# Kernel tuning notes

Measured on AMD Instinct MI355X. Metric: run time of the kernel, lower is better.

## Reference

```python
import jax, jax.numpy as jnp
import numpy as np


def setup_inputs() -> dict:
    key = jax.random.key(0)
    k1, k2, k3 = jax.random.split(key, 3)
    B, S, D, L = 8, 512, 512, 32
    head = jax.random.normal(k1, (B, S, D), dtype=jnp.float32)
    dep = jax.random.normal(k2, (B, S, D), dtype=jnp.float32)
    label_U_diag = jax.random.normal(k3, (L, D), dtype=jnp.float32)
    return {"head": head, "dep": dep, "label_U_diag": label_U_diag}


def reference(head, dep, label_U_diag):
    # head: [b, i, j], label_U_diag: [l, j], dep: [b, o, j] -> [b, l, i, o]
    return jnp.einsum('bij,lj,boj->blio', head, label_U_diag, dep)
```

## Files before the change

kernel.cpp:

```cpp
#include <hip/hip_runtime.h>
#include <hip/hip_bf16.h>

typedef float f32x4  __attribute__((ext_vector_type(4)));
typedef short bf16x8 __attribute__((ext_vector_type(8)));

__device__ __forceinline__ short bf16r(float x) {
    unsigned u = __builtin_bit_cast(unsigned, x);
    u += 0x7fffu + ((u >> 16) & 1u);
    return (short)(u >> 16);
}

__global__ void cvt_kernel(const float* __restrict__ head, const float* __restrict__ dep,
                           short* __restrict__ hb, short* __restrict__ db) {
    const int n8 = 8 * 512 * 512 / 8;
    int i = blockIdx.x * blockDim.x + threadIdx.x;
    const float* src = (i < n8) ? head : dep;
    short* dst = (i < n8) ? hb : db;
    int j = (i < n8) ? i : i - n8;
    f32x4 a = *(const f32x4*)(src + (size_t)j * 8);
    f32x4 c = *(const f32x4*)(src + (size_t)j * 8 + 4);
    bf16x8 v;
#pragma unroll
    for (int e = 0; e < 4; ++e) { v[e] = bf16r(a[e]); v[4 + e] = bf16r(c[e]); }
    *(bf16x8*)(dst + (size_t)j * 8) = v;
}

__global__ __launch_bounds__(512, 2)
void bla_gemm4(const short* __restrict__ headb,
               const short* __restrict__ depb,
               const float* __restrict__ U,
               float* __restrict__ out)
{
    constexpr int S = 512, D = 512, L = 32, BM = 256, BN = 256, BK = 64, NT = 8;

    __shared__ __align__(16) short Al[2][BM * BK];
    __shared__ __align__(16) short Bl[2][BN * BK];

    const int tid = threadIdx.x, lane = tid & 63, wid = tid >> 6;
    const int wm = wid >> 2, wn = wid & 3;

    const int swz = (blockIdx.x & 7) * ((int)gridDim.x >> 3) + (blockIdx.x >> 3);
    const int b = swz >> 7, rem = swz & 127;
    const int it = rem >> 6, l = (rem >> 1) & 31, ot = rem & 1;
    const int i0 = it * BM, o0 = ot * BN;

    const int ar = tid >> 3, ac = (tid & 7) * 8;
    const short* hbase = headb + (size_t)(b * S + i0 + ar) * D + ac;
    const float* ubase = U + (size_t)l * D + ac;
    const int awoff = ((((tid & 7) * 16) ^ ((ar & 7) << 4)) >> 1);

    const int bso = ((lane & 7) * 16) ^ ((lane >> 3) << 4);
    const short* dbase = depb + (size_t)(b * S + o0) * D;

    bf16x8 rA[2][4];
    f32x4  ru[2][2];

#define SBAR() __builtin_amdgcn_sched_barrier(0)

#define A_ISSUE(tt) do {                                                        \
        const int s_ = (tt) & 1;                                                \
        _Pragma("unroll")                                                       \
        for (int p = 0; p < 4; ++p)                                             \
            rA[s_][p] = *(const bf16x8*)(hbase + (size_t)(p * 64) * D + (tt) * BK); \
        ru[s_][0] = *(const f32x4*)(ubase + (tt) * BK);                         \
        ru[s_][1] = *(const f32x4*)(ubase + (tt) * BK + 4);                     \
    } while (0)

#define A_WRITE_H(tt, h) do {                                                   \
        const int s_ = (tt) & 1;                                                \
        _Pragma("unroll")                                                       \
        for (int p = (h) * 2; p < (h) * 2 + 2; ++p) {                           \
            bf16x8 av;                                                          \
            _Pragma("unroll")                                                   \
            for (int e = 0; e < 8; ++e) {                                       \
                float f = __builtin_bit_cast(float,                             \
                    (unsigned)((unsigned short)rA[s_][p][e]) << 16)             \
                    * ru[s_][e >> 2][e & 3];                                    \
                av[e] = __builtin_bit_cast(short, __float2bfloat16(f));         \
            }                                                                   \
            *(bf16x8*)&Al[s_][(ar + p * 64) * BK + awoff] = av;                 \
        }                                                                       \
    } while (0)

#define B_ISSUE_H(tt, h) do {                                                   \
        _Pragma("unroll")                                                       \
        for (int q = (h) * 2; q < (h) * 2 + 2; ++q) {                           \
            const int rg = wid * 32 + q * 8 + (lane >> 3);                      \
            const char* s_ = (const char*)dbase +                               \
                ((size_t)rg * D + (size_t)(tt) * BK) * 2 + bso;                 \
            __builtin_amdgcn_global_load_lds(                                   \
                (const __attribute__((address_space(1))) void*)s_,              \
                (__attribute__((address_space(3))) void*)&Bl[(tt) & 1][(wid * 32 + q * 8) * BK], \
                16, 0, 0);                                                      \
        }                                                                       \
    } while (0)

    f32x4 acc[8][4] = {};
    bf16x8 bfr[4];

#define DSREAD_A(buf_, mh_, ks_, af_) do {                                      \
        const int cb = (ks_) * 64 + ((lane >> 4) << 4);                         \
        _Pragma("unroll")                                                       \
        for (int f = 0; f < 4; ++f) {                                           \
            const int row = wm * 128 + ((mh_) * 4 + f) * 16 + (lane & 15);      \
            af_[f] = *(const bf16x8*)&Al[buf_][row * BK + ((cb ^ ((row & 7) << 4)) >> 1)]; \
        }                                                                       \
    } while (0)

#define DSREAD_B(buf_, ks_) do {                                                \
        const int cb = (ks_) * 64 + ((lane >> 4) << 4);                         \
        _Pragma("unroll")                                                       \
        for (int f = 0; f < 4; ++f) {                                           \
            const int row = wn * 64 + f * 16 + (lane & 15);                     \
            bfr[f] = *(const bf16x8*)&Bl[buf_][row * BK + ((cb ^ ((row & 7) << 4)) >> 1)]; \
        }                                                                       \
    } while (0)

#define MFMA16(mh_, af_) do {                                                   \
        __builtin_amdgcn_s_setprio(1);                                          \
        _Pragma("unroll")                                                       \
        for (int m = 0; m < 4; ++m)                                             \
            _Pragma("unroll")                                                   \
            for (int n = 0; n < 4; ++n)                                         \
                acc[(mh_) * 4 + m][n] = __builtin_amdgcn_mfma_f32_16x16x32_bf16(\
                    af_[m], bfr[n], acc[(mh_) * 4 + m][n], 0, 0, 0);            \
        __builtin_amdgcn_s_setprio(0);                                          \
    } while (0)

#define BAR() __builtin_amdgcn_s_barrier()

    A_ISSUE(0);
    B_ISSUE_H(0, 0); B_ISSUE_H(0, 1);
    SBAR();
    A_WRITE_H(0, 0); A_WRITE_H(0, 1);
    A_ISSUE(1);
    SBAR();
    asm volatile("s_waitcnt vmcnt(6) lgkmcnt(0)" ::: "memory");
    SBAR();
    BAR();
    SBAR();

#pragma unroll
    for (int t = 0; t < NT; ++t) {
        const int c = t & 1;
        bf16x8 af[4];

        DSREAD_A(c, 0, 0, af); DSREAD_B(c, 0);
        if (t + 1 < NT) B_ISSUE_H(t + 1, 0);
        SBAR(); BAR(); SBAR();
        MFMA16(0, af);
        SBAR(); BAR(); SBAR();

        DSREAD_A(c, 1, 0, af);
        if (t + 1 < NT) B_ISSUE_H(t + 1, 1);
        SBAR(); BAR(); SBAR();
        MFMA16(1, af);
        SBAR(); BAR(); SBAR();

        DSREAD_A(c, 0, 1, af); DSREAD_B(c, 1);
        if (t + 1 < NT) A_WRITE_H(t + 1, 0);
        SBAR(); BAR(); SBAR();
        MFMA16(0, af);
        SBAR(); BAR(); SBAR();

        DSREAD_A(c, 1, 1, af);
        if (t + 1 < NT) A_WRITE_H(t + 1, 1);
        if (t + 2 < NT) A_ISSUE(t + 2);
        SBAR(); BAR(); SBAR();
        MFMA16(1, af);
        SBAR();
        if (t + 2 < NT) {
            asm volatile("s_waitcnt vmcnt(6) lgkmcnt(0)" ::: "memory");
        } else if (t + 1 < NT) {
            asm volatile("s_waitcnt vmcnt(0) lgkmcnt(0)" ::: "memory");
        }
        SBAR(); BAR(); SBAR();
    }

    float* op = out + (size_t)(b * L + l) * S * S;
#pragma unroll
    for (int m = 0; m < 8; ++m) {
        const int row0 = i0 + wm * 128 + m * 16 + ((lane >> 4) << 2);
#pragma unroll
        for (int n = 0; n < 4; ++n) {
            const int col = o0 + wn * 64 + n * 16 + (lane & 15);
#pragma unroll
            for (int r = 0; r < 4; ++r)
                op[(size_t)(row0 + r) * S + col] = acc[m][n][r];
        }
    }

#undef SBAR
#undef A_ISSUE
#undef A_WRITE_H
#undef B_ISSUE_H
#undef DSREAD_A
#undef DSREAD_B
#undef MFMA16
#undef BAR
}

__global__ __launch_bounds__(256, 2)
void bla_fb(const float* __restrict__ head, const float* __restrict__ dep,
            const float* __restrict__ U, float* __restrict__ out)
{
    constexpr int S = 512, D = 512, L = 32, BM = 128, BN = 128, BK = 64, NT = 8;
    __shared__ short Al[2][BM * BK];
    __shared__ short Bl[2][BN * BK];
    const int tid = threadIdx.x, lane = tid & 63, wid = tid >> 6;
    const int wm = wid >> 1, wn = wid & 1;
    const int swz = (blockIdx.x & 7) * ((int)gridDim.x >> 3) + (blockIdx.x >> 3);
    const int b = swz >> 9, rem = swz & 511;
    const int l = rem >> 4, it = (rem >> 2) & 3, ot = rem & 3;
    const int i0 = it * BM, o0 = ot * BN;
    const int srow = tid >> 3, scol = (tid & 7) * 8, swb = scol * 2;
    const float* hb = head + (size_t)(b * S + i0 + srow) * D + scol;
    const float* db = dep + (size_t)(b * S + o0 + srow) * D + scol;
    const float* ub = U + l * D + scol;
    f32x4 ra[4][2], rb[4][2], ru[2];
#define FSTAGE_LOAD(t) do { const int k0_ = (t) * BK;                              \
        ru[0] = *(const f32x4*)(ub + k0_); ru[1] = *(const f32x4*)(ub + k0_ + 4);  \
        _Pragma("unroll") for (int p_ = 0; p_ < 4; ++p_) {                         \
            ra[p_][0] = *(const f32x4*)(hb + k0_ + p_ * 32 * D);                   \
            ra[p_][1] = *(const f32x4*)(hb + k0_ + p_ * 32 * D + 4);               \
            rb[p_][0] = *(const f32x4*)(db + k0_ + p_ * 32 * D);                   \
            rb[p_][1] = *(const f32x4*)(db + k0_ + p_ * 32 * D + 4); } } while (0)
#define FSTAGE_WRITE(buf) do { _Pragma("unroll") for (int p_ = 0; p_ < 4; ++p_) {  \
            const int row_ = srow + p_ * 32; const int sb_ = swb ^ ((row_ & 7) << 4); \
            bf16x8 av_, bv_;                                                       \
            _Pragma("unroll") for (int q_ = 0; q_ < 2; ++q_)                       \
                _Pragma("unroll") for (int j_ = 0; j_ < 4; ++j_) {                 \
                    av_[q_ * 4 + j_] = bf16r(ra[p_][q_][j_] * ru[q_][j_]);         \
                    bv_[q_ * 4 + j_] = bf16r(rb[p_][q_][j_]); }                    \
            *(bf16x8*)&Al[buf][row_ * BK + (sb_ >> 1)] = av_;                      \
            *(bf16x8*)&Bl[buf][row_ * BK + (sb_ >> 1)] = bv_; } } while (0)
    f32x4 acc[4][4] = {};
    const int cbase = (lane >> 4) << 4, rsw = (lane & 7) << 4;
#define FCOMPUTE(buf) do { _Pragma("unroll") for (int ks_ = 0; ks_ < 2; ++ks_) {   \
            const int sb2_ = (ks_ * 64 + cbase) ^ rsw; bf16x8 af_[4], bfr_[4];     \
            _Pragma("unroll") for (int f_ = 0; f_ < 4; ++f_) {                     \
                af_[f_] = *(const bf16x8*)&Al[buf][(wm * 64 + f_ * 16 + (lane & 15)) * BK + (sb2_ >> 1)]; \
                bfr_[f_] = *(const bf16x8*)&Bl[buf][(wn * 64 + f_ * 16 + (lane & 15)) * BK + (sb2_ >> 1)]; } \
            _Pragma("unroll") for (int fm_ = 0; fm_ < 4; ++fm_)                    \
                _Pragma("unroll") for (int fn_ = 0; fn_ < 4; ++fn_)                \
                    acc[fm_][fn_] = __builtin_amdgcn_mfma_f32_16x16x32_bf16(       \
                        af_[fm_], bfr_[fn_], acc[fm_][fn_], 0, 0, 0); } } while (0)
    FSTAGE_LOAD(0); FSTAGE_WRITE(0); __syncthreads();
    int cur = 0;
#pragma unroll
    for (int t = 0; t < NT; ++t) {
        if (t + 1 < NT) FSTAGE_LOAD(t + 1);
        FCOMPUTE(cur);
        if (t + 1 < NT) FSTAGE_WRITE(cur ^ 1);
        __syncthreads();
        cur ^= 1;
    }
    float* op = out + (size_t)(b * L + l) * S * S;
#pragma unroll
    for (int fm = 0; fm < 4; ++fm) {
        const int row0 = i0 + wm * 64 + fm * 16 + ((lane >> 4) << 2);
#pragma unroll
        for (int fn = 0; fn < 4; ++fn) {
            const int col = o0 + wn * 64 + fn * 16 + (lane & 15);
#pragma unroll
            for (int r = 0; r < 4; ++r)
                op[(size_t)(row0 + r) * S + col] = acc[fm][fn][r];
        }
    }
#undef FSTAGE_LOAD
#undef FSTAGE_WRITE
#undef FCOMPUTE
}

extern "C" void kernel_launch(void* const* d_in, const int* in_sizes, int n_in,
                              void* d_out, int out_size, void* d_ws, size_t ws_size,
                              hipStream_t stream)
{
    const float* head = (const float*)d_in[0];
    const float* dep  = (const float*)d_in[1];
    const float* U    = (const float*)d_in[2];
    float* out        = (float*)d_out;

    const size_t nelem = (size_t)8 * 512 * 512;
    const size_t need  = nelem * 2 * 2;
    if (ws_size >= need) {
        short* headb = (short*)d_ws;
        short* depb  = headb + nelem;
        cvt_kernel<<<dim3(2048), dim3(256), 0, stream>>>(head, dep, headb, depb);
        bla_gemm4<<<dim3(1024), dim3(512), 0, stream>>>(headb, depb, U, out);
    } else {
        bla_fb<<<dim3(4096), dim3(256), 0, stream>>>(head, dep, U, out);
    }
}
```

Measured before the change: 111.4 us.

## Shrink GEMM tiles to 128x128 with 256-thread blocks and l-innermost ordering

Replaces the 256x256 tile, 512-thread GEMM with a 128x128 tile, 256-thread variant launched on four times as many blocks. The block index decoding now puts the label dimension innermost, so neighbouring blocks share the same head and dep tiles, which should help L2 reuse. The pipeline is cut from four phases per K step to two, with the load and waitcnt counts adjusted to match. Smaller tiles mean less compute per byte moved and more total global traffic, in exchange for better occupancy and load balance.

```diff
diff --git a/kernel.cpp b/kernel.cpp
--- a/kernel.cpp
+++ b/kernel.cpp
@@ -25,66 +25,72 @@
     *(bf16x8*)(dst + (size_t)j * 8) = v;
 }
 
-__global__ __launch_bounds__(512, 2)
-void bla_gemm4(const short* __restrict__ headb,
+__global__ __launch_bounds__(256, 2)
+void bla_gemm5(const short* __restrict__ headb,
                const short* __restrict__ depb,
                const float* __restrict__ U,
                float* __restrict__ out)
 {
-    constexpr int S = 512, D = 512, L = 32, BM = 256, BN = 256, BK = 64, NT = 8;
+    constexpr int S = 512, D = 512, L = 32, BM = 128, BN = 128, BK = 64, NT = 8;
 
     __shared__ __align__(16) short Al[2][BM * BK];
     __shared__ __align__(16) short Bl[2][BN * BK];
 
     const int tid = threadIdx.x, lane = tid & 63, wid = tid >> 6;
-    const int wm = wid >> 2, wn = wid & 3;
+    const int wm = wid >> 1, wn = wid & 1;
 
     const int swz = (blockIdx.x & 7) * ((int)gridDim.x >> 3) + (blockIdx.x >> 3);
-    const int b = swz >> 7, rem = swz & 127;
-    const int it = rem >> 6, l = (rem >> 1) & 31, ot = rem & 1;
+    const int b = swz >> 9, rem = swz & 511;
+    const int it = rem >> 7, ot = (rem >> 5) & 3, l = rem & 31;
     const int i0 = it * BM, o0 = ot * BN;
 
-    const int ar = tid >> 3, ac = (tid & 7) * 8;
-    const short* hbase = headb + (size_t)(b * S + i0 + ar) * D + ac;
-    const float* ubase = U + (size_t)l * D + ac;
-    const int awoff = ((((tid & 7) * 16) ^ ((ar & 7) << 4)) >> 1);
+    const int arow = tid >> 2, acol = (tid & 3) * 16;
+    const short* hbase = headb + (size_t)(b * S + i0 + arow) * D + acol;
+    const float* ubase = U + (size_t)l * D + acol;
+    const int asw0 = (((acol * 2) ^ ((arow & 7) << 4)) >> 1);
+    const int asw1 = (((acol * 2 + 16) ^ ((arow & 7) << 4)) >> 1);
 
     const int bso = ((lane & 7) * 16) ^ ((lane >> 3) << 4);
     const short* dbase = depb + (size_t)(b * S + o0) * D;
 
     bf16x8 rA[2][4];
-    f32x4  ru[2][2];
+    f32x4  ru[2][4];
 
 #define SBAR() __builtin_amdgcn_sched_barrier(0)
+#define BAR()  __builtin_amdgcn_s_barrier()
 
 #define A_ISSUE(tt) do {                                                        \
         const int s_ = (tt) & 1;                                                \
         _Pragma("unroll")                                                       \
-        for (int p = 0; p < 4; ++p)                                             \
-            rA[s_][p] = *(const bf16x8*)(hbase + (size_t)(p * 64) * D + (tt) * BK); \
-        ru[s_][0] = *(const f32x4*)(ubase + (tt) * BK);                         \
-        ru[s_][1] = *(const f32x4*)(ubase + (tt) * BK + 4);                     \
-    } while (0)
-
-#define A_WRITE_H(tt, h) do {                                                   \
+        for (int p = 0; p < 2; ++p)                                             \
+            _Pragma("unroll")                                                   \
+            for (int q = 0; q < 2; ++q)                                         \
+                rA[s_][p * 2 + q] = *(const bf16x8*)(hbase +                    \
+                    (size_t)(p * 64) * D + (tt) * BK + q * 8);                  \
+        _Pragma("unroll")                                                       \
+        for (int j = 0; j < 4; ++j)                                             \
+            ru[s_][j] = *(const f32x4*)(ubase + (tt) * BK + j * 4);             \
+    } while (0)
+
+#define A_WRITE_P(tt, p) do {                                                   \
         const int s_ = (tt) & 1;                                                \
         _Pragma("unroll")                                                       \
-        for (int p = (h) * 2; p < (h) * 2 + 2; ++p) {                           \
+        for (int q = 0; q < 2; ++q) {                                           \
             bf16x8 av;                                                          \
             _Pragma("unroll")                                                   \
             for (int e = 0; e < 8; ++e) {                                       \
                 float f = __builtin_bit_cast(float,                             \
-                    (unsigned)((unsigned short)rA[s_][p][e]) << 16)             \
-                    * ru[s_][e >> 2][e & 3];                                    \
+                    (unsigned)((unsigned short)rA[s_][(p) * 2 + q][e]) << 16)   \
+                    * ru[s_][q * 2 + (e >> 2)][e & 3];                          \
                 av[e] = __builtin_bit_cast(short, __float2bfloat16(f));         \
             }                                                                   \
-            *(bf16x8*)&Al[s_][(ar + p * 64) * BK + awoff] = av;                 \
-        }                                                                       \
-    } while (0)
-
-#define B_ISSUE_H(tt, h) do {                                                   \
-        _Pragma("unroll")                                                       \
-        for (int q = (h) * 2; q < (h) * 2 + 2; ++q) {                           \
+            *(bf16x8*)&Al[s_][(arow + (p) * 64) * BK + (q ? asw1 : asw0)] = av; \
+        }                                                                       \
+    } while (0)
+
+#define B_ISSUE(tt) do {                                                        \
+        _Pragma("unroll")                                                       \
+        for (int q = 0; q < 4; ++q) {                                           \
             const int rg = wid * 32 + q * 8 + (lane >> 3);                      \
             const char* s_ = (const char*)dbase +                               \
                 ((size_t)rg * D + (size_t)(tt) * BK) * 2 + bso;                 \
@@ -95,14 +101,14 @@
         }                                                                       \
     } while (0)
 
-    f32x4 acc[8][4] = {};
+    f32x4 acc[4][4] = {};
     bf16x8 bfr[4];
 
-#define DSREAD_A(buf_, mh_, ks_, af_) do {                                      \
+#define DSREAD_A(buf_, ks_, af_) do {                                           \
         const int cb = (ks_) * 64 + ((lane >> 4) << 4);                         \
         _Pragma("unroll")                                                       \
         for (int f = 0; f < 4; ++f) {                                           \
-            const int row = wm * 128 + ((mh_) * 4 + f) * 16 + (lane & 15);      \
+            const int row = wm * 64 + f * 16 + (lane & 15);                     \
             af_[f] = *(const bf16x8*)&Al[buf_][row * BK + ((cb ^ ((row & 7) << 4)) >> 1)]; \
         }                                                                       \
     } while (0)
@@ -116,26 +122,24 @@
         }                                                                       \
     } while (0)
 
-#define MFMA16(mh_, af_) do {                                                   \
+#define MFMA16(af_) do {                                                        \
         __builtin_amdgcn_s_setprio(1);                                          \
         _Pragma("unroll")                                                       \
         for (int m = 0; m < 4; ++m)                                             \
             _Pragma("unroll")                                                   \
             for (int n = 0; n < 4; ++n)                                         \
-                acc[(mh_) * 4 + m][n] = __builtin_amdgcn_mfma_f32_16x16x32_bf16(\
-                    af_[m], bfr[n], acc[(mh_) * 4 + m][n], 0, 0, 0);            \
+                acc[m][n] = __builtin_amdgcn_mfma_f32_16x16x32_bf16(            \
+                    af_[m], bfr[n], acc[m][n], 0, 0, 0);                        \
         __builtin_amdgcn_s_setprio(0);                                          \
     } while (0)
 
-#define BAR() __builtin_amdgcn_s_barrier()
-
     A_ISSUE(0);
-    B_ISSUE_H(0, 0); B_ISSUE_H(0, 1);
-    SBAR();
-    A_WRITE_H(0, 0); A_WRITE_H(0, 1);
+    B_ISSUE(0);
+    SBAR();
+    A_WRITE_P(0, 0); A_WRITE_P(0, 1);
     A_ISSUE(1);
     SBAR();
-    asm volatile("s_waitcnt vmcnt(6) lgkmcnt(0)" ::: "memory");
+    asm volatile("s_waitcnt vmcnt(8) lgkmcnt(0)" ::: "memory");
     SBAR();
     BAR();
     SBAR();
@@ -145,32 +149,20 @@
         const int c = t & 1;
         bf16x8 af[4];
 
-        DSREAD_A(c, 0, 0, af); DSREAD_B(c, 0);
-        if (t + 1 < NT) B_ISSUE_H(t + 1, 0);
-        SBAR(); BAR(); SBAR();
-        MFMA16(0, af);
-        SBAR(); BAR(); SBAR();
-
-        DSREAD_A(c, 1, 0, af);
-        if (t + 1 < NT) B_ISSUE_H(t + 1, 1);
-        SBAR(); BAR(); SBAR();
-        MFMA16(1, af);
-        SBAR(); BAR(); SBAR();
-
-        DSREAD_A(c, 0, 1, af); DSREAD_B(c, 1);
-        if (t + 1 < NT) A_WRITE_H(t + 1, 0);
-        SBAR(); BAR(); SBAR();
-        MFMA16(0, af);
-        SBAR(); BAR(); SBAR();
-
-        DSREAD_A(c, 1, 1, af);
-        if (t + 1 < NT) A_WRITE_H(t + 1, 1);
+        DSREAD_A(c, 0, af); DSREAD_B(c, 0);
+        if (t + 1 < NT) { B_ISSUE(t + 1); A_WRITE_P(t + 1, 0); }
+        SBAR(); BAR(); SBAR();
+        MFMA16(af);
+        SBAR(); BAR(); SBAR();
+
+        DSREAD_A(c, 1, af); DSREAD_B(c, 1);
+        if (t + 1 < NT) A_WRITE_P(t + 1, 1);
         if (t + 2 < NT) A_ISSUE(t + 2);
         SBAR(); BAR(); SBAR();
-        MFMA16(1, af);
+        MFMA16(af);
         SBAR();
         if (t + 2 < NT) {
-            asm volatile("s_waitcnt vmcnt(6) lgkmcnt(0)" ::: "memory");
+            asm volatile("s_waitcnt vmcnt(8) lgkmcnt(0)" ::: "memory");
         } else if (t + 1 < NT) {
             asm volatile("s_waitcnt vmcnt(0) lgkmcnt(0)" ::: "memory");
         }
@@ -179,8 +171,8 @@
 
     float* op = out + (size_t)(b * L + l) * S * S;
 #pragma unroll
-    for (int m = 0; m < 8; ++m) {
-        const int row0 = i0 + wm * 128 + m * 16 + ((lane >> 4) << 2);
+    for (int m = 0; m < 4; ++m) {
+        const int row0 = i0 + wm * 64 + m * 16 + ((lane >> 4) << 2);
 #pragma unroll
         for (int n = 0; n < 4; ++n) {
             const int col = o0 + wn * 64 + n * 16 + (lane & 15);
@@ -191,13 +183,13 @@
     }
 
 #undef SBAR
+#undef BAR
 #undef A_ISSUE
-#undef A_WRITE_H
-#undef B_ISSUE_H
+#undef A_WRITE_P
+#undef B_ISSUE
 #undef DSREAD_A
 #undef DSREAD_B
 #undef MFMA16
-#undef BAR
 }
 
 __global__ __launch_bounds__(256, 2)
@@ -287,7 +279,7 @@
         short* headb = (short*)d_ws;
         short* depb  = headb + nelem;
         cvt_kernel<<<dim3(2048), dim3(256), 0, stream>>>(head, dep, headb, depb);
-        bla_gemm4<<<dim3(1024), dim3(512), 0, stream>>>(headb, depb, U, out);
+        bla_gemm5<<<dim3(4096), dim3(256), 0, stream>>>(headb, depb, U, out);
     } else {
         bla_fb<<<dim3(4096), dim3(256), 0, stream>>>(head, dep, U, out);
     }
```

After: 131.4 us. 17.9% more time.

## Precompute head*U per label into workspace and load both GEMM operands via LDS-direct

Applied to the files above, without the earlier changes.

A prep kernel now writes a bf16 copy of head scaled by U for every label, plus bf16 dep, into workspace. This materialised tensor is 32x larger than head. The GEMM then streams both A and B tiles with global_load_lds, which removes the register-staged scaling and LDS writes from the main loop and simplifies its waits. Block order is remapped so that blocks sharing the same dep tile run next to each other. The trade-off is a large extra HBM write in the prep stage, and A-tile reads with no reuse across labels. If the workspace is too small, the code falls back to the unfused kernel.

```diff
diff --git a/kernel.cpp b/kernel.cpp
--- a/kernel.cpp
+++ b/kernel.cpp
@@ -10,26 +10,42 @@
     return (short)(u >> 16);
 }
 
-__global__ void cvt_kernel(const float* __restrict__ head, const float* __restrict__ dep,
-                           short* __restrict__ hb, short* __restrict__ db) {
-    const int n8 = 8 * 512 * 512 / 8;
-    int i = blockIdx.x * blockDim.x + threadIdx.x;
-    const float* src = (i < n8) ? head : dep;
-    short* dst = (i < n8) ? hb : db;
-    int j = (i < n8) ? i : i - n8;
-    f32x4 a = *(const f32x4*)(src + (size_t)j * 8);
-    f32x4 c = *(const f32x4*)(src + (size_t)j * 8 + 4);
-    bf16x8 v;
-#pragma unroll
-    for (int e = 0; e < 4; ++e) { v[e] = bf16r(a[e]); v[4 + e] = bf16r(c[e]); }
-    *(bf16x8*)(dst + (size_t)j * 8) = v;
+__global__ void prep_kernel(const float* __restrict__ head, const float* __restrict__ dep,
+                            const float* __restrict__ U,
+                            short* __restrict__ hs, short* __restrict__ dp) {
+    const int NH = 8 * 32 * 512 * 64;
+    int gid = blockIdx.x * blockDim.x + threadIdx.x;
+    if (gid < NH) {
+        const int k8 = gid & 63;
+        const int i  = (gid >> 6) & 511;
+        const int l  = (gid >> 15) & 31;
+        const int b  = gid >> 20;
+        const float* hsrc = head + ((size_t)(b * 512 + i)) * 512 + k8 * 8;
+        const float* usrc = U + (size_t)l * 512 + k8 * 8;
+        f32x4 h0 = *(const f32x4*)hsrc,      h1 = *(const f32x4*)(hsrc + 4);
+        f32x4 u0 = *(const f32x4*)usrc,      u1 = *(const f32x4*)(usrc + 4);
+        bf16x8 v;
+#pragma unroll
+        for (int e = 0; e < 4; ++e) {
+            v[e]     = bf16r(h0[e] * u0[e]);
+            v[4 + e] = bf16r(h1[e] * u1[e]);
+        }
+        *(bf16x8*)(hs + (((size_t)(b * 32 + l) * 512 + i) * 512 + k8 * 8)) = v;
+    } else {
+        const int j = gid - NH;
+        f32x4 a = *(const f32x4*)(dep + (size_t)j * 8);
+        f32x4 c = *(const f32x4*)(dep + (size_t)j * 8 + 4);
+        bf16x8 v;
+#pragma unroll
+        for (int e = 0; e < 4; ++e) { v[e] = bf16r(a[e]); v[4 + e] = bf16r(c[e]); }
+        *(bf16x8*)(dp + (size_t)j * 8) = v;
+    }
 }
 
 __global__ __launch_bounds__(512, 2)
-void bla_gemm4(const short* __restrict__ headb,
-               const short* __restrict__ depb,
-               const float* __restrict__ U,
-               float* __restrict__ out)
+void bla_gemm12(const short* __restrict__ hs,
+                const short* __restrict__ dp,
+                float* __restrict__ out)
 {
     constexpr int S = 512, D = 512, L = 32, BM = 256, BN = 256, BK = 64, NT = 8;
 
@@ -41,56 +57,38 @@
 
     const int swz = (blockIdx.x & 7) * ((int)gridDim.x >> 3) + (blockIdx.x >> 3);
     const int b = swz >> 7, rem = swz & 127;
-    const int it = rem >> 6, l = (rem >> 1) & 31, ot = rem & 1;
+    const int it = rem >> 6, ot = (rem >> 5) & 1, l = rem & 31;
     const int i0 = it * BM, o0 = ot * BN;
 
-    const int ar = tid >> 3, ac = (tid & 7) * 8;
-    const short* hbase = headb + (size_t)(b * S + i0 + ar) * D + ac;
-    const float* ubase = U + (size_t)l * D + ac;
-    const int awoff = ((((tid & 7) * 16) ^ ((ar & 7) << 4)) >> 1);
-
     const int bso = ((lane & 7) * 16) ^ ((lane >> 3) << 4);
-    const short* dbase = depb + (size_t)(b * S + o0) * D;
-
-    bf16x8 rA[2][4];
-    f32x4  ru[2][2];
+    const char* asrc = (const char*)(hs + ((size_t)(b * 32 + l) * 512 + i0) * D) + bso;
+    const char* bsrc = (const char*)(dp + (size_t)(b * S + o0) * D) + bso;
 
 #define SBAR() __builtin_amdgcn_sched_barrier(0)
-
-#define A_ISSUE(tt) do {                                                        \
-        const int s_ = (tt) & 1;                                                \
-        _Pragma("unroll")                                                       \
-        for (int p = 0; p < 4; ++p)                                             \
-            rA[s_][p] = *(const bf16x8*)(hbase + (size_t)(p * 64) * D + (tt) * BK); \
-        ru[s_][0] = *(const f32x4*)(ubase + (tt) * BK);                         \
-        ru[s_][1] = *(const f32x4*)(ubase + (tt) * BK + 4);                     \
-    } while (0)
-
-#define A_WRITE_H(tt, h) do {                                                   \
-        const int s_ = (tt) & 1;                                                \
-        _Pragma("unroll")                                                       \
-        for (int p = (h) * 2; p < (h) * 2 + 2; ++p) {                           \
-            bf16x8 av;                                                          \
-            _Pragma("unroll")                                                   \
-            for (int e = 0; e < 8; ++e) {                                       \
-                float f = __builtin_bit_cast(float,                             \
-                    (unsigned)((unsigned short)rA[s_][p][e]) << 16)             \
-                    * ru[s_][e >> 2][e & 3];                                    \
-                av[e] = __builtin_bit_cast(short, __float2bfloat16(f));         \
-            }                                                                   \
-            *(bf16x8*)&Al[s_][(ar + p * 64) * BK + awoff] = av;                 \
-        }                                                                       \
-    } while (0)
-
-#define B_ISSUE_H(tt, h) do {                                                   \
-        _Pragma("unroll")                                                       \
-        for (int q = (h) * 2; q < (h) * 2 + 2; ++q) {                           \
-            const int rg = wid * 32 + q * 8 + (lane >> 3);                      \
-            const char* s_ = (const char*)dbase +                               \
-                ((size_t)rg * D + (size_t)(tt) * BK) * 2 + bso;                 \
+#define BAR()  __builtin_amdgcn_s_barrier()
+
+#define A_GLOAD(tt) do {                                                        \
+        _Pragma("unroll")                                                       \
+        for (int q = 0; q < 4; ++q) {                                           \
+            const int rg = q * 64 + wid * 8 + (lane >> 3);                      \
             __builtin_amdgcn_global_load_lds(                                   \
-                (const __attribute__((address_space(1))) void*)s_,              \
-                (__attribute__((address_space(3))) void*)&Bl[(tt) & 1][(wid * 32 + q * 8) * BK], \
+                (const __attribute__((address_space(1))) void*)(asrc +          \
+                    ((size_t)rg * D + (size_t)(tt) * BK) * 2),                  \
+                (__attribute__((address_space(3))) void*)                       \
+                    (&Al[(tt) & 1][(q * 64 + wid * 8) * BK] + lane * 8),        \
+                16, 0, 0);                                                      \
+        }                                                                       \
+    } while (0)
+
+#define B_GLOAD(tt) do {                                                        \
+        _Pragma("unroll")                                                       \
+        for (int q = 0; q < 4; ++q) {                                           \
+            const int rg = q * 64 + wid * 8 + (lane >> 3);                      \
+            __builtin_amdgcn_global_load_lds(                                   \
+                (const __attribute__((address_space(1))) void*)(bsrc +          \
+                    ((size_t)rg * D + (size_t)(tt) * BK) * 2),                  \
+                (__attribute__((address_space(3))) void*)                       \
+                    (&Bl[(tt) & 1][(q * 64 + wid * 8) * BK] + lane * 8),        \
                 16, 0, 0);                                                      \
         }                                                                       \
     } while (0)
@@ -127,15 +125,10 @@
         __builtin_amdgcn_s_setprio(0);                                          \
     } while (0)
 
-#define BAR() __builtin_amdgcn_s_barrier()
-
-    A_ISSUE(0);
-    B_ISSUE_H(0, 0); B_ISSUE_H(0, 1);
+    A_GLOAD(0);
+    B_GLOAD(0);
     SBAR();
-    A_WRITE_H(0, 0); A_WRITE_H(0, 1);
-    A_ISSUE(1);
-    SBAR();
-    asm volatile("s_waitcnt vmcnt(6) lgkmcnt(0)" ::: "memory");
+    asm volatile("s_waitcnt vmcnt(0) lgkmcnt(0)" ::: "memory");
     SBAR();
     BAR();
     SBAR();
@@ -146,35 +139,32 @@
         bf16x8 af[4];
 
         DSREAD_A(c, 0, 0, af); DSREAD_B(c, 0);
-        if (t + 1 < NT) B_ISSUE_H(t + 1, 0);
+        if (t + 1 < NT) A_GLOAD(t + 1);
         SBAR(); BAR(); SBAR();
         MFMA16(0, af);
         SBAR(); BAR(); SBAR();
 
         DSREAD_A(c, 1, 0, af);
-        if (t + 1 < NT) B_ISSUE_H(t + 1, 1);
+        if (t + 1 < NT) B_GLOAD(t + 1);
         SBAR(); BAR(); SBAR();
         MFMA16(1, af);
         SBAR(); BAR(); SBAR();
 
         DSREAD_A(c, 0, 1, af); DSREAD_B(c, 1);
-        if (t + 1 < NT) A_WRITE_H(t + 1, 0);
         SBAR(); BAR(); SBAR();
         MFMA16(0, af);
         SBAR(); BAR(); SBAR();
 
         DSREAD_A(c, 1, 1, af);
-        if (t + 1 < NT) A_WRITE_H(t + 1, 1);
-        if (t + 2 < NT) A_ISSUE(t + 2);
         SBAR(); BAR(); SBAR();
         MFMA16(1, af);
         SBAR();
-        if (t + 2 < NT) {
-            asm volatile("s_waitcnt vmcnt(6) lgkmcnt(0)" ::: "memory");
-        } else if (t + 1 < NT) {
-            asm volatile("s_waitcnt vmcnt(0) lgkmcnt(0)" ::: "memory");
-        }
-        SBAR(); BAR(); SBAR();
+        if (t + 1 < NT) {
+            asm volatile("s_waitcnt vmcnt(0)" ::: "memory");
+            SBAR();
+            BAR();
+            SBAR();
+        }
     }
 
     float* op = out + (size_t)(b * L + l) * S * S;
@@ -191,13 +181,12 @@
     }
 
 #undef SBAR
-#undef A_ISSUE
-#undef A_WRITE_H
-#undef B_ISSUE_H
+#undef BAR
+#undef A_GLOAD
+#undef B_GLOAD
 #undef DSREAD_A
 #undef DSREAD_B
 #undef MFMA16
-#undef BAR
 }
 
 __global__ __launch_bounds__(256, 2)
@@ -281,13 +270,14 @@
     const float* U    = (const float*)d_in[2];
     float* out        = (float*)d_out;
 
-    const size_t nelem = (size_t)8 * 512 * 512;
-    const size_t need  = nelem * 2 * 2;
+    const size_t nhs  = (size_t)8 * 32 * 512 * 512;
+    const size_t ndep = (size_t)8 * 512 * 512;
+    const size_t need = (nhs + ndep) * 2;
     if (ws_size >= need) {
-        short* headb = (short*)d_ws;
-        short* depb  = headb + nelem;
-        cvt_kernel<<<dim3(2048), dim3(256), 0, stream>>>(head, dep, headb, depb);
-        bla_gemm4<<<dim3(1024), dim3(512), 0, stream>>>(headb, depb, U, out);
+        short* hs = (short*)d_ws;
+        short* dp = hs + nhs;
+        prep_kernel<<<dim3(33792), dim3(256), 0, stream>>>(head, dep, U, hs, dp);
+        bla_gemm12<<<dim3(1024), dim3(512), 0, stream>>>(hs, dp, out);
     } else {
         bla_fb<<<dim3(4096), dim3(256), 0, stream>>>(head, dep, U, out);
     }
```

New measurement: 156.9 us. +40.8%, slower.
